# Kernel optimization log

Hardware: AMD Instinct MI355X
Metric: run time of the kernel (lower is better)

Reference implementation:

```python
import jax, jax.numpy as jnp
import numpy as np

THRESHOLD_SCALE = 0.75
EPS = 1e-6


def setup_inputs() -> dict:
    key = jax.random.key(0)
    k1, k2 = jax.random.split(key)
    B, IN, OUT = 8192, 4096, 4096
    x = jax.random.normal(k1, (B, IN), dtype=jnp.float32)
    # xavier_uniform-like init, then clip to [-1, 1] as clip_weights_ would
    bound = float(np.sqrt(6.0 / (IN + OUT)))
    weight = jax.random.uniform(k2, (OUT, IN), dtype=jnp.float32, minval=-bound, maxval=bound)
    bias = jnp.zeros((OUT,), dtype=jnp.float32)
    return {"x": x, "weight": weight, "bias": bias}


def reference(x, weight, bias):
    # per-output-row scale (detached in torch -> stop_gradient)
    scale = jax.lax.stop_gradient(
        jnp.maximum(jnp.mean(jnp.abs(weight), axis=1, keepdims=True), EPS)
    )  # [out, 1]
    threshold = scale * THRESHOLD_SCALE
    # ternary quantize: {-1, 0, +1}
    q = jnp.where(weight >= threshold, 1.0, jnp.where(weight <= -threshold, -1.0, 0.0)).astype(weight.dtype)
    # STE: forward = q, backward passes grad through where |w| <= 1
    mask = (jnp.abs(weight) <= 1.0).astype(weight.dtype)
    q_ste = weight * mask + jax.lax.stop_gradient(q - weight * mask)
    w_eff = q_ste * scale  # [out, in]
    return x @ w_eff.T + bias
```

## Files before the change

### kernel.cpp

```cpp
#include <hip/hip_runtime.h>
#include <hip/hip_bf16.h>

typedef __attribute__((ext_vector_type(4))) int i32x4;

#define GLOBAL_CAST(p) (const __attribute__((address_space(1))) void*)(p)
#define LDS_CAST(p)    (__attribute__((address_space(3))) void*)(p)

__global__ __launch_bounds__(256) void scale_quant_kernel(
    const float* __restrict__ w, float* __restrict__ scale,
    signed char* __restrict__ q, int K)
{
    const int row = blockIdx.x;
    const int tid = threadIdx.x;
    const float* wrow = w + (size_t)row * K;
    const int nvec = K >> 2;
    const float4* wv = (const float4*)wrow;

    __shared__ float red[4];
    const int lane = tid & 63, wid = tid >> 6;

    if (nvec == 1024) {
        float4 v[4];
        float s = 0.f;
        #pragma unroll
        for (int j = 0; j < 4; ++j) {
            v[j] = wv[tid + j * 256];
            s += fabsf(v[j].x) + fabsf(v[j].y) + fabsf(v[j].z) + fabsf(v[j].w);
        }
        #pragma unroll
        for (int off = 32; off > 0; off >>= 1) s += __shfl_down(s, off);
        if (lane == 0) red[wid] = s;
        __syncthreads();
        const float total = red[0] + red[1] + red[2] + red[3];
        const float sc = fmaxf(total / (float)K, 1e-6f);
        const float thr = sc * 0.75f;
        if (tid == 0) scale[row] = sc;
        if (q != nullptr) {
            char4* qv = (char4*)(q + (size_t)row * K);
            #pragma unroll
            for (int j = 0; j < 4; ++j) {
                char4 o;
                o.x = (v[j].x >= thr) ? 1 : ((v[j].x <= -thr) ? -1 : 0);
                o.y = (v[j].y >= thr) ? 1 : ((v[j].y <= -thr) ? -1 : 0);
                o.z = (v[j].z >= thr) ? 1 : ((v[j].z <= -thr) ? -1 : 0);
                o.w = (v[j].w >= thr) ? 1 : ((v[j].w <= -thr) ? -1 : 0);
                qv[tid + j * 256] = o;
            }
        }
        return;
    }

    float s = 0.f;
    for (int i = tid; i < nvec; i += blockDim.x) {
        float4 v = wv[i];
        s += fabsf(v.x) + fabsf(v.y) + fabsf(v.z) + fabsf(v.w);
    }
    #pragma unroll
    for (int off = 32; off > 0; off >>= 1) s += __shfl_down(s, off);
    if (lane == 0) red[wid] = s;
    __syncthreads();
    const float total = red[0] + red[1] + red[2] + red[3];
    const float sc = fmaxf(total / (float)K, 1e-6f);
    const float thr = sc * 0.75f;
    if (tid == 0) scale[row] = sc;
    if (q != nullptr) {
        char4* qv = (char4*)(q + (size_t)row * K);
        for (int i = tid; i < nvec; i += blockDim.x) {
            float4 v = wv[i];
            char4 o;
            o.x = (v.x >= thr) ? 1 : ((v.x <= -thr) ? -1 : 0);
            o.y = (v.y >= thr) ? 1 : ((v.y <= -thr) ? -1 : 0);
            o.z = (v.z >= thr) ? 1 : ((v.z <= -thr) ? -1 : 0);
            o.w = (v.w >= thr) ? 1 : ((v.w <= -thr) ? -1 : 0);
            qv[i] = o;
        }
    }
}

__global__ __launch_bounds__(256) void x_quant_kernel(
    const float* __restrict__ x, float* __restrict__ sx,
    signed char* __restrict__ xq, int K)
{
    const int row = blockIdx.x;
    const int tid = threadIdx.x;
    const float4* xv = (const float4*)(x + (size_t)row * K);
    const int nvec = K >> 2;

    __shared__ float red[4];
    const int lane = tid & 63, wid = tid >> 6;

    if (nvec == 1024) {
        float4 v[4];
        float am = 0.f;
        #pragma unroll
        for (int j = 0; j < 4; ++j) {
            v[j] = xv[tid + j * 256];
            am = fmaxf(am, fmaxf(fmaxf(fabsf(v[j].x), fabsf(v[j].y)),
                                 fmaxf(fabsf(v[j].z), fabsf(v[j].w))));
        }
        #pragma unroll
        for (int off = 32; off > 0; off >>= 1) am = fmaxf(am, __shfl_down(am, off));
        if (lane == 0) red[wid] = am;
        __syncthreads();
        const float amax = fmaxf(fmaxf(red[0], red[1]), fmaxf(red[2], red[3]));
        const float inv = (amax > 0.f) ? (127.f / amax) : 0.f;
        if (tid == 0) sx[row] = amax * (1.f / 127.f);
        char4* qv = (char4*)(xq + (size_t)row * K);
        #pragma unroll
        for (int j = 0; j < 4; ++j) {
            char4 o;
            o.x = (signed char)__float2int_rn(v[j].x * inv);
            o.y = (signed char)__float2int_rn(v[j].y * inv);
            o.z = (signed char)__float2int_rn(v[j].z * inv);
            o.w = (signed char)__float2int_rn(v[j].w * inv);
            qv[tid + j * 256] = o;
        }
        return;
    }

    float am = 0.f;
    for (int i = tid; i < nvec; i += blockDim.x) {
        float4 v = xv[i];
        am = fmaxf(am, fmaxf(fmaxf(fabsf(v.x), fabsf(v.y)), fmaxf(fabsf(v.z), fabsf(v.w))));
    }
    #pragma unroll
    for (int off = 32; off > 0; off >>= 1) am = fmaxf(am, __shfl_down(am, off));
    if (lane == 0) red[wid] = am;
    __syncthreads();
    const float amax = fmaxf(fmaxf(red[0], red[1]), fmaxf(red[2], red[3]));
    const float inv = (amax > 0.f) ? (127.f / amax) : 0.f;
    if (tid == 0) sx[row] = amax * (1.f / 127.f);
    char4* qv = (char4*)(xq + (size_t)row * K);
    for (int i = tid; i < nvec; i += blockDim.x) {
        float4 v = xv[i];
        char4 o;
        o.x = (signed char)__float2int_rn(v.x * inv);
        o.y = (signed char)__float2int_rn(v.y * inv);
        o.z = (signed char)__float2int_rn(v.z * inv);
        o.w = (signed char)__float2int_rn(v.w * inv);
        qv[i] = o;
    }
}

#define BM 256
#define BN 256
#define BK 128

__global__ __launch_bounds__(512, 2) void gemm256_i8_kernel(
    const signed char* __restrict__ Xq,
    const signed char* __restrict__ Qq,
    const float* __restrict__ sx,
    const float* __restrict__ scale,
    const float* __restrict__ bias,
    float* __restrict__ out, int M, int N, int K)
{
    __shared__ __align__(16) char lds[131072];

    const int tid  = threadIdx.x;
    const int lane = tid & 63;
    const int wid  = tid >> 6;
    const int wm   = wid >> 2;
    const int wn   = wid & 3;
    const int kh   = lane >> 4;
    const int lr   = lane & 15;
    const int grp  = wm;

    int bid = blockIdx.x;
    const int nwg = gridDim.x;
    if ((nwg & 7) == 0) { const int cpx = nwg >> 3; bid = (bid & 7) * cpx + (bid >> 3); }
    const int nbn = N / BN;
    const int tm = bid / nbn, tn = bid % nbn;
    const int arow0 = tm * BM;
    const int brow0 = tn * BN;
    const int NT = K / BK;

    unsigned aoff[8], boff[4];
    #pragma unroll
    for (int mf = 0; mf < 8; ++mf) {
        const int row = wm * 128 + mf * 16 + lr;
        aoff[mf] = (unsigned)(row * 128 + ((kh ^ (row & 7)) << 4));
    }
    #pragma unroll
    for (int nf = 0; nf < 4; ++nf) {
        const int row = wn * 64 + nf * 16 + lr;
        boff[nf] = (unsigned)(32768 + row * 128 + ((kh ^ (row & 7)) << 4));
    }

    const int r0 = tid >> 3;
    const int c0 = (((tid & 7) ^ (r0 & 7)) << 4);
    const int ci1 = 512 + tid;
    const int r1 = ci1 >> 3;
    const int c1 = (((ci1 & 7) ^ (r1 & 7)) << 4);

    const signed char* asrc[2][2];
    const signed char* bsrc[2][2];
    unsigned adst[2][2], bdst[2][2];
    #pragma unroll
    for (int hh = 0; hh < 2; ++hh) {
        asrc[hh][0] = Xq + (size_t)(arow0 + hh * 128 + r0) * K + BK + c0;
        asrc[hh][1] = Xq + (size_t)(arow0 + hh * 128 + r1) * K + BK + c1;
        bsrc[hh][0] = Qq + (size_t)(brow0 + hh * 128 + r0) * K + BK + c0;
        bsrc[hh][1] = Qq + (size_t)(brow0 + hh * 128 + r1) * K + BK + c1;
        adst[hh][0] = (unsigned)(hh * 16384 + tid * 16);
        adst[hh][1] = (unsigned)(hh * 16384 + ci1 * 16);
        bdst[hh][0] = (unsigned)(32768 + hh * 16384 + tid * 16);
        bdst[hh][1] = (unsigned)(32768 + hh * 16384 + ci1 * 16);
    }

    #pragma unroll
    for (int hh = 0; hh < 2; ++hh) {
        const int rowA = arow0 + hh * 128, rowB = brow0 + hh * 128;
        const signed char* ga0 = Xq + (size_t)(rowA + r0) * K + c0;
        const signed char* ga1 = Xq + (size_t)(rowA + r1) * K + c1;
        const signed char* gb0 = Qq + (size_t)(rowB + r0) * K + c0;
        const signed char* gb1 = Qq + (size_t)(rowB + r1) * K + c1;
        __builtin_amdgcn_global_load_lds(GLOBAL_CAST(ga0), LDS_CAST(lds + adst[hh][0]), 16, 0, 0);
        __builtin_amdgcn_global_load_lds(GLOBAL_CAST(ga1), LDS_CAST(lds + adst[hh][1]), 16, 0, 0);
        __builtin_amdgcn_global_load_lds(GLOBAL_CAST(gb0), LDS_CAST(lds + bdst[hh][0]), 16, 0, 0);
        __builtin_amdgcn_global_load_lds(GLOBAL_CAST(gb1), LDS_CAST(lds + bdst[hh][1]), 16, 0, 0);
    }
    asm volatile("s_waitcnt vmcnt(0)" ::: "memory");
    __builtin_amdgcn_sched_barrier(0);
    __builtin_amdgcn_s_barrier();

    i32x4 acc[8][4] = {};
    i32x4 a[8], b[4];

    #define PHASE(KX)                                                          \
        _Pragma("unroll")                                                      \
        for (int nf = 0; nf < 4; ++nf)                                         \
            b[nf] = *(const i32x4*)(lds + ((tb | boff[nf]) ^ (KX)));           \
        _Pragma("unroll")                                                      \
        for (int mf = 0; mf < 8; ++mf)                                         \
            a[mf] = *(const i32x4*)(lds + ((tb | aoff[mf]) ^ (KX)));           \
        __builtin_amdgcn_s_setprio(1);                                         \
        _Pragma("unroll")                                                      \
        for (int mf = 0; mf < 8; ++mf)                                         \
            _Pragma("unroll")                                                  \
            for (int nf = 0; nf < 4; ++nf)                                     \
                acc[mf][nf] = __builtin_amdgcn_mfma_i32_16x16x64_i8(           \
                    a[mf], b[nf], acc[mf][nf], 0, 0, 0);                       \
        __builtin_amdgcn_s_setprio(0);

    const unsigned kx0 = (unsigned)grp << 6;
    const unsigned kx1 = kx0 ^ 64u;

    for (int t = 0; t < NT; ++t) {
        const unsigned tb = (unsigned)(t & 1) << 16;
        const unsigned ta = tb ^ 0x10000u;
        const bool doS = (t < NT - 1);

        if (doS) {
            #pragma unroll
            for (int hh = 0; hh < 2; ++hh) {
                __builtin_amdgcn_global_load_lds(GLOBAL_CAST(asrc[hh][0]), LDS_CAST(lds + (ta | adst[hh][0])), 16, 0, 0);
                __builtin_amdgcn_global_load_lds(GLOBAL_CAST(asrc[hh][1]), LDS_CAST(lds + (ta | adst[hh][1])), 16, 0, 0);
            }
        }
        PHASE(kx0)

        if (doS) {
            #pragma unroll
            for (int hh = 0; hh < 2; ++hh) {
                __builtin_amdgcn_global_load_lds(GLOBAL_CAST(bsrc[hh][0]), LDS_CAST(lds + (ta | bdst[hh][0])), 16, 0, 0);
                __builtin_amdgcn_global_load_lds(GLOBAL_CAST(bsrc[hh][1]), LDS_CAST(lds + (ta | bdst[hh][1])), 16, 0, 0);
            }
        }
        PHASE(kx1)

        #pragma unroll
        for (int hh = 0; hh < 2; ++hh) {
            asrc[hh][0] += BK; asrc[hh][1] += BK;
            bsrc[hh][0] += BK; bsrc[hh][1] += BK;
        }
        asm volatile("s_waitcnt vmcnt(0)" ::: "memory");
        __builtin_amdgcn_sched_barrier(0);
        __builtin_amdgcn_s_barrier();
    }
    #undef PHASE

    float sxv[32];
    #pragma unroll
    for (int mf = 0; mf < 8; ++mf)
        #pragma unroll
        for (int r = 0; r < 4; ++r)
            sxv[mf * 4 + r] = sx[arow0 + wm * 128 + mf * 16 + kh * 4 + r];

    #pragma unroll
    for (int nf = 0; nf < 4; ++nf) {
        const int gn = brow0 + wn * 64 + nf * 16 + lr;
        const float sc = scale[gn];
        const float bs = bias[gn];
        #pragma unroll
        for (int mf = 0; mf < 8; ++mf) {
            const size_t gm = (size_t)arow0 + wm * 128 + mf * 16 + kh * 4;
            #pragma unroll
            for (int r = 0; r < 4; ++r)
                out[(gm + r) * (size_t)N + gn] =
                    (float)acc[mf][nf][r] * (sxv[mf * 4 + r] * sc) + bs;
        }
    }
}

__global__ __launch_bounds__(256) void fb_gemm_kernel(
    const float* __restrict__ X, const float* __restrict__ W,
    const float* __restrict__ scale, const float* __restrict__ bias,
    float* __restrict__ out, int M, int N, int K)
{
    __shared__ float xs[16][16];
    __shared__ float qs[16][17];
    const int tx = threadIdx.x & 15, ty = threadIdx.x >> 4;
    const int m = blockIdx.y * 16 + ty;
    const int n = blockIdx.x * 16 + tx;
    const int nrow = blockIdx.x * 16 + ty;
    const int mL = min(m, M - 1);
    const int nrowL = min(nrow, N - 1);
    const float thr = scale[nrowL] * 0.75f;
    float acc = 0.f;
    for (int k0 = 0; k0 < K; k0 += 16) {
        xs[ty][tx] = X[(size_t)mL * K + k0 + tx];
        const float w = W[(size_t)nrowL * K + k0 + tx];
        qs[ty][tx] = (w >= thr) ? 1.f : ((w <= -thr) ? -1.f : 0.f);
        __syncthreads();
        #pragma unroll
        for (int kk = 0; kk < 16; ++kk) acc += xs[ty][kk] * qs[tx][kk];
        __syncthreads();
    }
    if (m < M && n < N) out[(size_t)m * N + n] = scale[n] * acc + bias[n];
}

extern "C" void kernel_launch(void* const* d_in, const int* in_sizes, int n_in,
                              void* d_out, int out_size, void* d_ws, size_t ws_size,
                              hipStream_t stream)
{
    const float* x    = (const float*)d_in[0];
    const float* w    = (const float*)d_in[1];
    const float* bias = (const float*)d_in[2];
    float* out = (float*)d_out;

    const int N = in_sizes[2];
    const int K = in_sizes[1] / N;
    const int M = in_sizes[0] / K;

    const size_t scOff = 0;
    const size_t sxOff = (scOff + (size_t)N * 4 + 255) & ~(size_t)255;
    const size_t qOff  = (sxOff + (size_t)M * 4 + 255) & ~(size_t)255;
    const size_t xqOff = (qOff + (size_t)N * K + 255) & ~(size_t)255;
    const size_t need  = xqOff + (size_t)M * K;

    float* scale = (float*)((char*)d_ws + scOff);

    const bool fast = (ws_size >= need) &&
                      (M % BM == 0) && (N % BN == 0) && (K % BK == 0) &&
                      ((K & 3) == 0) && (K / BK >= 4) &&
                      (((M / BM) * (N / BN)) % 8 == 0);

    if (fast) {
        float* sx        = (float*)((char*)d_ws + sxOff);
        signed char* q   = (signed char*)((char*)d_ws + qOff);
        signed char* xq  = (signed char*)((char*)d_ws + xqOff);

        scale_quant_kernel<<<N, 256, 0, stream>>>(w, scale, q, K);
        x_quant_kernel<<<M, 256, 0, stream>>>(x, sx, xq, K);

        const int grid = (M / BM) * (N / BN);
        gemm256_i8_kernel<<<grid, 512, 0, stream>>>(xq, q, sx, scale, bias, out, M, N, K);
    } else {
        scale_quant_kernel<<<N, 256, 0, stream>>>(w, scale, nullptr, K);
        dim3 g((N + 15) / 16, (M + 15) / 16);
        fb_gemm_kernel<<<g, 256, 0, stream>>>(x, w, scale, bias, out, M, N, K);
    }
}
```

Baseline: 180.4 us.

## Use five-slot LDS ring of 64-wide K slices with deeper prefetch

Replaces the double-buffered 128-wide K tile with a ring of five 32 KB LDS slots, each holding a 64-byte K slice of A and B, prefetched up to three slices ahead. The wait only requires the older loads to finish (vmcnt(4)), so global-to-LDS copies overlap more compute. LDS use grows to 160 KB and launch bounds drop to one workgroup per CU, which reduces occupancy. The swizzle is reworked for 64-byte rows.

```diff
diff --git a/kernel.cpp b/kernel.cpp
--- a/kernel.cpp
+++ b/kernel.cpp
@@ -145,8 +145,10 @@
 #define BM 256
 #define BN 256
 #define BK 128
-
-__global__ __launch_bounds__(512, 2) void gemm256_i8_kernel(
+#define REG 32768u
+#define LDS5 163840u
+
+__global__ __launch_bounds__(512, 1) void gemm256_i8_kernel(
     const signed char* __restrict__ Xq,
     const signed char* __restrict__ Qq,
     const float* __restrict__ sx,
@@ -154,7 +156,7 @@
     const float* __restrict__ bias,
     float* __restrict__ out, int M, int N, int K)
 {
-    __shared__ __align__(16) char lds[131072];
+    __shared__ __align__(16) char lds[LDS5];
 
     const int tid  = threadIdx.x;
     const int lane = tid & 63;
@@ -163,7 +165,6 @@
     const int wn   = wid & 3;
     const int kh   = lane >> 4;
     const int lr   = lane & 15;
-    const int grp  = wm;
 
     int bid = blockIdx.x;
     const int nwg = gridDim.x;
@@ -178,46 +179,36 @@
     #pragma unroll
     for (int mf = 0; mf < 8; ++mf) {
         const int row = wm * 128 + mf * 16 + lr;
-        aoff[mf] = (unsigned)(row * 128 + ((kh ^ (row & 7)) << 4));
+        aoff[mf] = (unsigned)(row * 64 + ((kh ^ ((row >> 1) & 3)) << 4));
     }
     #pragma unroll
     for (int nf = 0; nf < 4; ++nf) {
         const int row = wn * 64 + nf * 16 + lr;
-        boff[nf] = (unsigned)(32768 + row * 128 + ((kh ^ (row & 7)) << 4));
-    }
-
-    const int r0 = tid >> 3;
-    const int c0 = (((tid & 7) ^ (r0 & 7)) << 4);
-    const int ci1 = 512 + tid;
-    const int r1 = ci1 >> 3;
-    const int c1 = (((ci1 & 7) ^ (r1 & 7)) << 4);
-
-    const signed char* asrc[2][2];
-    const signed char* bsrc[2][2];
-    unsigned adst[2][2], bdst[2][2];
-    #pragma unroll
-    for (int hh = 0; hh < 2; ++hh) {
-        asrc[hh][0] = Xq + (size_t)(arow0 + hh * 128 + r0) * K + BK + c0;
-        asrc[hh][1] = Xq + (size_t)(arow0 + hh * 128 + r1) * K + BK + c1;
-        bsrc[hh][0] = Qq + (size_t)(brow0 + hh * 128 + r0) * K + BK + c0;
-        bsrc[hh][1] = Qq + (size_t)(brow0 + hh * 128 + r1) * K + BK + c1;
-        adst[hh][0] = (unsigned)(hh * 16384 + tid * 16);
-        adst[hh][1] = (unsigned)(hh * 16384 + ci1 * 16);
-        bdst[hh][0] = (unsigned)(32768 + hh * 16384 + tid * 16);
-        bdst[hh][1] = (unsigned)(32768 + hh * 16384 + ci1 * 16);
-    }
-
-    #pragma unroll
-    for (int hh = 0; hh < 2; ++hh) {
-        const int rowA = arow0 + hh * 128, rowB = brow0 + hh * 128;
-        const signed char* ga0 = Xq + (size_t)(rowA + r0) * K + c0;
-        const signed char* ga1 = Xq + (size_t)(rowA + r1) * K + c1;
-        const signed char* gb0 = Qq + (size_t)(rowB + r0) * K + c0;
-        const signed char* gb1 = Qq + (size_t)(rowB + r1) * K + c1;
-        __builtin_amdgcn_global_load_lds(GLOBAL_CAST(ga0), LDS_CAST(lds + adst[hh][0]), 16, 0, 0);
-        __builtin_amdgcn_global_load_lds(GLOBAL_CAST(ga1), LDS_CAST(lds + adst[hh][1]), 16, 0, 0);
-        __builtin_amdgcn_global_load_lds(GLOBAL_CAST(gb0), LDS_CAST(lds + bdst[hh][0]), 16, 0, 0);
-        __builtin_amdgcn_global_load_lds(GLOBAL_CAST(gb1), LDS_CAST(lds + bdst[hh][1]), 16, 0, 0);
+        boff[nf] = 16384u + (unsigned)(row * 64 + ((kh ^ ((row >> 1) & 3)) << 4));
+    }
+
+    const int rA0 = tid >> 2, sA0 = tid & 3;
+    const int colA0 = (sA0 ^ ((rA0 >> 1) & 3)) << 4;
+    const int rA1 = rA0 + 128;
+    const int colA1 = (sA0 ^ ((rA1 >> 1) & 3)) << 4;
+    const unsigned dA0 = (unsigned)(tid * 16);
+    const unsigned dA1 = (unsigned)((tid + 512) * 16);
+    const unsigned dB0 = 16384u + dA0;
+    const unsigned dB1 = 16384u + dA1;
+
+    const signed char* aS0 = Xq + (size_t)(arow0 + rA0) * K + colA0;
+    const signed char* aS1 = Xq + (size_t)(arow0 + rA1) * K + colA1;
+    const signed char* bS0 = Qq + (size_t)(brow0 + rA0) * K + colA0;
+    const signed char* bS1 = Qq + (size_t)(brow0 + rA1) * K + colA1;
+
+    #pragma unroll
+    for (int rho = 0; rho < 3; ++rho) {
+        const unsigned sb = (unsigned)rho * REG;
+        __builtin_amdgcn_global_load_lds(GLOBAL_CAST(aS0), LDS_CAST(lds + (sb | dA0)), 16, 0, 0);
+        __builtin_amdgcn_global_load_lds(GLOBAL_CAST(aS1), LDS_CAST(lds + (sb | dA1)), 16, 0, 0);
+        __builtin_amdgcn_global_load_lds(GLOBAL_CAST(bS0), LDS_CAST(lds + (sb | dB0)), 16, 0, 0);
+        __builtin_amdgcn_global_load_lds(GLOBAL_CAST(bS1), LDS_CAST(lds + (sb | dB1)), 16, 0, 0);
+        aS0 += 64; aS1 += 64; bS0 += 64; bS1 += 64;
     }
     asm volatile("s_waitcnt vmcnt(0)" ::: "memory");
     __builtin_amdgcn_sched_barrier(0);
@@ -226,13 +217,13 @@
     i32x4 acc[8][4] = {};
     i32x4 a[8], b[4];
 
-    #define PHASE(KX)                                                          \
+    #define PHASE(RB)                                                          \
         _Pragma("unroll")                                                      \
         for (int nf = 0; nf < 4; ++nf)                                         \
-            b[nf] = *(const i32x4*)(lds + ((tb | boff[nf]) ^ (KX)));           \
+            b[nf] = *(const i32x4*)(lds + ((RB) + boff[nf]));                  \
         _Pragma("unroll")                                                      \
         for (int mf = 0; mf < 8; ++mf)                                         \
-            a[mf] = *(const i32x4*)(lds + ((tb | aoff[mf]) ^ (KX)));           \
+            a[mf] = *(const i32x4*)(lds + ((RB) + aoff[mf]));                  \
         __builtin_amdgcn_s_setprio(1);                                         \
         _Pragma("unroll")                                                      \
         for (int mf = 0; mf < 8; ++mf)                                         \
@@ -242,42 +233,44 @@
                     a[mf], b[nf], acc[mf][nf], 0, 0, 0);                       \
         __builtin_amdgcn_s_setprio(0);
 
-    const unsigned kx0 = (unsigned)grp << 6;
-    const unsigned kx1 = kx0 ^ 64u;
+    #define STAGE(SB) {                                                        \
+        __builtin_amdgcn_global_load_lds(GLOBAL_CAST(aS0), LDS_CAST(lds + ((SB) | dA0)), 16, 0, 0); \
+        __builtin_amdgcn_global_load_lds(GLOBAL_CAST(aS1), LDS_CAST(lds + ((SB) | dA1)), 16, 0, 0); \
+        __builtin_amdgcn_global_load_lds(GLOBAL_CAST(bS0), LDS_CAST(lds + ((SB) | dB0)), 16, 0, 0); \
+        __builtin_amdgcn_global_load_lds(GLOBAL_CAST(bS1), LDS_CAST(lds + ((SB) | dB1)), 16, 0, 0); \
+        aS0 += 64; aS1 += 64; bS0 += 64; bS1 += 64;                            \
+        __builtin_amdgcn_sched_barrier(0); }
+
+    unsigned base0 = 0u;
+    unsigned base1 = REG;
+    unsigned sbase = 3u * REG;
+    const int NPH = 2 * NT;
 
     for (int t = 0; t < NT; ++t) {
-        const unsigned tb = (unsigned)(t & 1) << 16;
-        const unsigned ta = tb ^ 0x10000u;
-        const bool doS = (t < NT - 1);
-
-        if (doS) {
-            #pragma unroll
-            for (int hh = 0; hh < 2; ++hh) {
-                __builtin_amdgcn_global_load_lds(GLOBAL_CAST(asrc[hh][0]), LDS_CAST(lds + (ta | adst[hh][0])), 16, 0, 0);
-                __builtin_amdgcn_global_load_lds(GLOBAL_CAST(asrc[hh][1]), LDS_CAST(lds + (ta | adst[hh][1])), 16, 0, 0);
-            }
-        }
-        PHASE(kx0)
-
-        if (doS) {
-            #pragma unroll
-            for (int hh = 0; hh < 2; ++hh) {
-                __builtin_amdgcn_global_load_lds(GLOBAL_CAST(bsrc[hh][0]), LDS_CAST(lds + (ta | bdst[hh][0])), 16, 0, 0);
-                __builtin_amdgcn_global_load_lds(GLOBAL_CAST(bsrc[hh][1]), LDS_CAST(lds + (ta | bdst[hh][1])), 16, 0, 0);
-            }
-        }
-        PHASE(kx1)
-
-        #pragma unroll
-        for (int hh = 0; hh < 2; ++hh) {
-            asrc[hh][0] += BK; asrc[hh][1] += BK;
-            bsrc[hh][0] += BK; bsrc[hh][1] += BK;
-        }
-        asm volatile("s_waitcnt vmcnt(0)" ::: "memory");
+        const unsigned rbF = wm ? base1 : base0;
+        const unsigned rbS = wm ? base0 : base1;
+
+        if (2 * t + 3 < NPH) {
+            STAGE(sbase)
+            sbase += REG; if (sbase >= LDS5) sbase = 0u;
+        }
+        PHASE(rbF)
+
+        if (2 * t + 4 < NPH) {
+            STAGE(sbase)
+            sbase += REG; if (sbase >= LDS5) sbase = 0u;
+        }
+        PHASE(rbS)
+
+        base0 += 2u * REG; if (base0 >= LDS5) base0 -= LDS5;
+        base1 = base0 + REG; if (base1 >= LDS5) base1 -= LDS5;
+        if (t < NT - 2) { asm volatile("s_waitcnt vmcnt(4)" ::: "memory"); }
+        else            { asm volatile("s_waitcnt vmcnt(0)" ::: "memory"); }
         __builtin_amdgcn_sched_barrier(0);
         __builtin_amdgcn_s_barrier();
     }
     #undef PHASE
+    #undef STAGE
 
     float sxv[32];
     #pragma unroll
```

After: 189.9 us. 5.3% more time.
